# Optimization experiments

Measured on AMD Instinct MI355X. Metric: run time of the kernel, lower is better.

The kernel has to match this reference:

```python
import jax, jax.numpy as jnp
import numpy as np

BATCH = 1024
D = 256          # input_size == embed_size (forced by elementwise multiply)
NUM_REL = 42     # num_classes + 2
FEAT = 30


def setup_inputs() -> dict:
    key = jax.random.key(0)
    k_x, k_q, k_f, k_r = jax.random.split(key, 4)
    x = jax.random.normal(k_x, (BATCH, D), dtype=jnp.float32)
    x_mask = jnp.ones((BATCH,), dtype=bool)  # unused by the module body
    q = jax.random.randint(k_q, (BATCH, BATCH), 0, NUM_REL, dtype=jnp.int64)
    f = jax.random.normal(k_f, (BATCH, FEAT), dtype=jnp.float32)  # unused by the module body
    # relation embedding table, init std=0.001, row 0 zeroed (padding relation)
    R_emb = jax.random.normal(k_r, (NUM_REL, D), dtype=jnp.float32) * 0.001
    R_emb = R_emb.at[0].set(0.0)
    return {"x": x, "x_mask": x_mask, "q": q, "f": f, "R_emb": R_emb}


def reference(x, x_mask, q, f, R_emb):
    # r[i,j,d] = R_emb[q[i,j], d]   (the big O(B^2*D) gather)
    r = R_emb[q]  # [B, B, D]
    # attn[i,j] = sum_d r[i,j,d] * x[j,d] * x[i,d]
    attn = jnp.einsum('ijd,jd,id->ij', r, x, x)  # [B, B]
    weights = jax.nn.softmax(attn, axis=-1)
    outputs = weights @ x  # [B, D]
    return outputs
```

## Files before the change

kernel.cpp:

```cpp
#include <hip/hip_runtime.h>
#include <hip/hip_bf16.h>

#define BB 1024
#define DD 256
#define NREL 42
#define AST 264

typedef __attribute__((ext_vector_type(8))) short short8_t;
typedef __attribute__((ext_vector_type(4))) short short4_t;
typedef __attribute__((ext_vector_type(4))) float f32x4;
typedef __attribute__((ext_vector_type(4))) int   i32x4;
typedef __attribute__((ext_vector_type(4))) unsigned int u32x4;

__device__ __forceinline__ unsigned short bf16_of(float f) {
    unsigned u = __float_as_uint(f);
    return (unsigned short)((u + 0x7FFFu + ((u >> 16) & 1u)) >> 16);
}

__device__ __forceinline__ float blo(unsigned u) { return __uint_as_float(u << 16); }
__device__ __forceinline__ float bhi(unsigned u) { return __uint_as_float(u & 0xFFFF0000u); }

__device__ __forceinline__ void dot8bf4(u32x4 a0, u32x4 a1, u32x4 a2, u32x4 a3,
                                        u32x4 xv,
                                        float& r0, float& r1, float& r2, float& r3) {
    #pragma unroll
    for (int e = 0; e < 4; ++e) {
        const float xl = blo(xv[e]);
        const float xh = bhi(xv[e]);
        r0 = fmaf(blo(a0[e]), xl, r0);  r0 = fmaf(bhi(a0[e]), xh, r0);
        r1 = fmaf(blo(a1[e]), xl, r1);  r1 = fmaf(bhi(a1[e]), xh, r1);
        r2 = fmaf(blo(a2[e]), xl, r2);  r2 = fmaf(bhi(a2[e]), xh, r2);
        r3 = fmaf(blo(a3[e]), xl, r3);  r3 = fmaf(bhi(a3[e]), xh, r3);
    }
}

__global__ __launch_bounds__(256) void cvt_kernel(const float* __restrict__ x,
                                                  unsigned short* __restrict__ xh8,
                                                  unsigned short* __restrict__ xbfT) {
    __shared__ float t32[64][68];
    const int bj = blockIdx.x * 64;
    const int bd = blockIdx.y * 64;
    const int tid = threadIdx.x;
    const int tr = tid >> 4;
    const int tc = tid & 15;

    #pragma unroll
    for (int rr = 0; rr < 4; ++rr) {
        const int jl = rr * 16 + tr;
        const f32x4 v = *reinterpret_cast<const f32x4*>(&x[(bj + jl) * DD + bd + tc * 4]);
        *reinterpret_cast<f32x4*>(&t32[jl][tc * 4]) = v;
    }
    __syncthreads();

    #pragma unroll
    for (int rr = 0; rr < 4; ++rr) {
        const int dl = rr * 16 + tr;
        short4_t h;
        #pragma unroll
        for (int e = 0; e < 4; ++e) h[e] = (short)bf16_of(t32[tc * 4 + e][dl]);
        *reinterpret_cast<short4_t*>(&xbfT[(bd + dl) * BB + bj + tc * 4]) = h;
    }

    #pragma unroll
    for (int c = 0; c < 2; ++c) {
        const int idx = c * 256 + tid;
        const int jl  = idx & 63;
        const int d8l = idx >> 6;
        short8_t hv;
        #pragma unroll
        for (int e = 0; e < 8; ++e) hv[e] = (short)bf16_of(t32[jl][d8l * 8 + e]);
        *reinterpret_cast<short8_t*>(
            &xh8[(size_t)((bd >> 3) + d8l) * (BB * 8) + (bj + jl) * 8]) = hv;
    }
}

__global__ __launch_bounds__(1024) void attn_kernel(const float* __restrict__ x,
                                                    const int* __restrict__ q,
                                                    const float* __restrict__ R,
                                                    const unsigned short* __restrict__ xh8,
                                                    unsigned short* __restrict__ P) {
    __shared__ __align__(16) unsigned short Ah[4][NREL * AST];
    __shared__ float s_attn[4][BB];
    __shared__ unsigned short s_qs[4][BB];

    const int tid  = threadIdx.x;
    const int w    = tid >> 6;
    const int lane = tid & 63;
    const int i0   = blockIdx.x * 4;

    {
        const int r  = tid >> 8;
        const int c4 = (tid & 255) * 4;
        const int qi = i0 + r;
        const i32x4 qa = *reinterpret_cast<const i32x4*>(&q[qi * BB + c4]);
        short4_t sa;
        sa[0] = (short)qa[0]; sa[1] = (short)qa[1];
        sa[2] = (short)qa[2]; sa[3] = (short)qa[3];
        *reinterpret_cast<short4_t*>(&s_qs[r][c4]) = sa;
    }

    #pragma unroll
    for (int i2 = 0; i2 < 4; ++i2) {
        const int i = i0 + i2;
        for (int c = tid; c < NREL * 32; c += 1024) {
            const int k  = c >> 5;
            const int d0 = (c & 31) * 8;
            const f32x4 r0 = *reinterpret_cast<const f32x4*>(&R[k * DD + d0]);
            const f32x4 r1 = *reinterpret_cast<const f32x4*>(&R[k * DD + d0 + 4]);
            const f32x4 x0 = *reinterpret_cast<const f32x4*>(&x[i * DD + d0]);
            const f32x4 x1 = *reinterpret_cast<const f32x4*>(&x[i * DD + d0 + 4]);
            short8_t hv;
            #pragma unroll
            for (int e = 0; e < 4; ++e) {
                hv[e]     = (short)bf16_of(r0[e] * x0[e]);
                hv[e + 4] = (short)bf16_of(r1[e] * x1[e]);
            }
            *reinterpret_cast<short8_t*>(&Ah[i2][k * AST + d0]) = hv;
        }
    }

    __syncthreads();

    const int j0 = tid;
    const unsigned short* a0 = &Ah[0][(int)s_qs[0][j0] * AST];
    const unsigned short* a1 = &Ah[1][(int)s_qs[1][j0] * AST];
    const unsigned short* a2 = &Ah[2][(int)s_qs[2][j0] * AST];
    const unsigned short* a3 = &Ah[3][(int)s_qs[3][j0] * AST];
    const unsigned short* xp = xh8 + (size_t)j0 * 8;

    float c0 = 0.f, c1 = 0.f, c2 = 0.f, c3 = 0.f;

    #pragma unroll 2
    for (int d8 = 0; d8 < 32; ++d8) {
        const u32x4 xv = *reinterpret_cast<const u32x4*>(xp + (size_t)d8 * (BB * 8));

        const int ao = d8 * 8;
        const u32x4 av0 = *reinterpret_cast<const u32x4*>(a0 + ao);
        const u32x4 av1 = *reinterpret_cast<const u32x4*>(a1 + ao);
        const u32x4 av2 = *reinterpret_cast<const u32x4*>(a2 + ao);
        const u32x4 av3 = *reinterpret_cast<const u32x4*>(a3 + ao);

        dot8bf4(av0, av1, av2, av3, xv, c0, c1, c2, c3);
    }

    s_attn[0][j0] = c0;
    s_attn[1][j0] = c1;
    s_attn[2][j0] = c2;
    s_attn[3][j0] = c3;

    __syncthreads();

    const int p2 = w >> 2;
    const int jq = w & 3;
    const int i  = i0 + p2;

    f32x4 v4[4];
    #pragma unroll
    for (int kk = 0; kk < 4; ++kk)
        v4[kk] = *reinterpret_cast<const f32x4*>(&s_attn[p2][kk * 256 + lane * 4]);

    float m = -1e30f;
    #pragma unroll
    for (int kk = 0; kk < 4; ++kk)
        m = fmaxf(m, fmaxf(fmaxf(v4[kk][0], v4[kk][1]), fmaxf(v4[kk][2], v4[kk][3])));
    #pragma unroll
    for (int off = 1; off < 64; off <<= 1) m = fmaxf(m, __shfl_xor(m, off));

    float e[16];
    float ssum = 0.f;
    #pragma unroll
    for (int kk = 0; kk < 4; ++kk)
        #pragma unroll
        for (int ee = 0; ee < 4; ++ee) {
            const float t2 = __expf(v4[kk][ee] - m);
            e[kk * 4 + ee] = t2;
            ssum += t2;
        }
    #pragma unroll
    for (int off = 1; off < 64; off <<= 1) ssum += __shfl_xor(ssum, off);
    const float inv = 1.0f / ssum;

    {
        short4_t pv;
        #pragma unroll
        for (int ee = 0; ee < 4; ++ee) pv[ee] = (short)bf16_of(e[jq * 4 + ee] * inv);
        *reinterpret_cast<short4_t*>(&P[i * BB + jq * 256 + lane * 4]) = pv;
    }
}

__global__ __launch_bounds__(256) void out_partial(const unsigned short* __restrict__ P,
                                                   const unsigned short* __restrict__ xbfT,
                                                   float* __restrict__ part) {
    const int tid = threadIdx.x;
    const int wave = tid >> 6, lane = tid & 63;
    const int lcol = lane & 15;
    const int lk8  = (lane >> 4) * 8;
    const int i0 = blockIdx.y * 64 + wave * 16;
    const int d0 = blockIdx.x * 64;
    const int k0 = blockIdx.z * 256;

    f32x4 acc[4];
    #pragma unroll
    for (int nt = 0; nt < 4; ++nt) acc[nt] = (f32x4)0.0f;

    #pragma unroll
    for (int ks = 0; ks < 8; ++ks) {
        const short8_t a = *reinterpret_cast<const short8_t*>(
            &P[(i0 + lcol) * BB + k0 + ks * 32 + lk8]);
        #pragma unroll
        for (int nt = 0; nt < 4; ++nt) {
            const short8_t b = *reinterpret_cast<const short8_t*>(
                &xbfT[(d0 + nt * 16 + lcol) * BB + k0 + ks * 32 + lk8]);
            acc[nt] = __builtin_amdgcn_mfma_f32_16x16x32_bf16(a, b, acc[nt], 0, 0, 0);
        }
    }

    const int rbase = (lane >> 4) * 4;
    float* pz = part + (size_t)blockIdx.z * BB * DD;
    #pragma unroll
    for (int r = 0; r < 4; ++r)
        #pragma unroll
        for (int nt = 0; nt < 4; ++nt)
            pz[(i0 + rbase + r) * DD + d0 + nt * 16 + lcol] = acc[nt][r];
}

__global__ __launch_bounds__(256) void out_reduce(const float* __restrict__ part,
                                                  float* __restrict__ out) {
    const int idx = blockIdx.x * DD + threadIdx.x;
    out[idx] = (part[idx] + part[BB * DD + idx]) +
               (part[2 * BB * DD + idx] + part[3 * BB * DD + idx]);
}

extern "C" void kernel_launch(void* const* d_in, const int* in_sizes, int n_in,
                              void* d_out, int out_size, void* d_ws, size_t ws_size,
                              hipStream_t stream) {
    (void)in_sizes; (void)n_in; (void)out_size; (void)ws_size;
    const float* x = (const float*)d_in[0];
    const int* q = (const int*)d_in[2];
    const float* R = (const float*)d_in[4];
    float* out = (float*)d_out;

    char* ws = (char*)d_ws;
    unsigned short* xh8  = (unsigned short*)(ws);
    unsigned short* xbfT = (unsigned short*)(ws + (512u << 10));
    unsigned short* P    = (unsigned short*)(ws + (1024u << 10));
    float*          part = (float*)(ws + (3072u << 10));

    cvt_kernel<<<dim3(16, 4), 256, 0, stream>>>(x, xh8, xbfT);
    attn_kernel<<<dim3(256), 1024, 0, stream>>>(x, q, R, xh8, P);
    out_partial<<<dim3(4, 16, 4), 256, 0, stream>>>(P, xbfT, part);
    out_reduce<<<dim3(BB), 256, 0, stream>>>(part, out);
}
```

Measured before the change: 40.71 us.

## Process two query rows per attention block and split softmax across waves

The attention kernel now handles two rows per block instead of four, so it launches twice as many blocks and uses half the shared memory per block. The aim is more parallelism across the 256 compute units and more blocks resident at once. Each row's softmax is now spread over 8 waves, with cross-wave max and sum reductions through shared memory, adding two extra barriers. The trade-off is that every xh8 column load is reused for only two rows rather than four, which doubles global traffic for x and for the per-block Ah table setup.

```diff
diff --git a/kernel.cpp b/kernel.cpp
--- a/kernel.cpp
+++ b/kernel.cpp
@@ -8,8 +8,11 @@
 
 typedef __attribute__((ext_vector_type(8))) short short8_t;
 typedef __attribute__((ext_vector_type(4))) short short4_t;
+typedef __attribute__((ext_vector_type(2))) short short2_t;
 typedef __attribute__((ext_vector_type(4))) float f32x4;
+typedef __attribute__((ext_vector_type(2))) float f32x2;
 typedef __attribute__((ext_vector_type(4))) int   i32x4;
+typedef __attribute__((ext_vector_type(2))) int   i32x2;
 typedef __attribute__((ext_vector_type(4))) unsigned int u32x4;
 
 __device__ __forceinline__ unsigned short bf16_of(float f) {
@@ -20,17 +23,16 @@
 __device__ __forceinline__ float blo(unsigned u) { return __uint_as_float(u << 16); }
 __device__ __forceinline__ float bhi(unsigned u) { return __uint_as_float(u & 0xFFFF0000u); }
 
-__device__ __forceinline__ void dot8bf4(u32x4 a0, u32x4 a1, u32x4 a2, u32x4 a3,
-                                        u32x4 xv,
-                                        float& r0, float& r1, float& r2, float& r3) {
+__device__ __forceinline__ void dot8bf2(u32x4 aa, u32x4 ab, u32x4 xv,
+                                        float& ra, float& rb) {
     #pragma unroll
     for (int e = 0; e < 4; ++e) {
         const float xl = blo(xv[e]);
         const float xh = bhi(xv[e]);
-        r0 = fmaf(blo(a0[e]), xl, r0);  r0 = fmaf(bhi(a0[e]), xh, r0);
-        r1 = fmaf(blo(a1[e]), xl, r1);  r1 = fmaf(bhi(a1[e]), xh, r1);
-        r2 = fmaf(blo(a2[e]), xl, r2);  r2 = fmaf(bhi(a2[e]), xh, r2);
-        r3 = fmaf(blo(a3[e]), xl, r3);  r3 = fmaf(bhi(a3[e]), xh, r3);
+        ra = fmaf(blo(aa[e]), xl, ra);
+        ra = fmaf(bhi(aa[e]), xh, ra);
+        rb = fmaf(blo(ab[e]), xl, rb);
+        rb = fmaf(bhi(ab[e]), xh, rb);
     }
 }
 
@@ -79,28 +81,27 @@
                                                     const float* __restrict__ R,
                                                     const unsigned short* __restrict__ xh8,
                                                     unsigned short* __restrict__ P) {
-    __shared__ __align__(16) unsigned short Ah[4][NREL * AST];
-    __shared__ float s_attn[4][BB];
-    __shared__ unsigned short s_qs[4][BB];
+    __shared__ __align__(16) unsigned short Ah[2][NREL * AST];
+    __shared__ float s_attn[2][BB];
+    __shared__ unsigned short s_qs[2][BB];
+    __shared__ float red_m[2][8], red_s[2][8];
 
     const int tid  = threadIdx.x;
     const int w    = tid >> 6;
     const int lane = tid & 63;
-    const int i0   = blockIdx.x * 4;
+    const int i0   = blockIdx.x * 2;
 
     {
-        const int r  = tid >> 8;
-        const int c4 = (tid & 255) * 4;
-        const int qi = i0 + r;
-        const i32x4 qa = *reinterpret_cast<const i32x4*>(&q[qi * BB + c4]);
-        short4_t sa;
+        const int r  = tid >> 9;
+        const int c2 = (tid & 511) * 2;
+        const i32x2 qa = *reinterpret_cast<const i32x2*>(&q[(i0 + r) * BB + c2]);
+        short2_t sa;
         sa[0] = (short)qa[0]; sa[1] = (short)qa[1];
-        sa[2] = (short)qa[2]; sa[3] = (short)qa[3];
-        *reinterpret_cast<short4_t*>(&s_qs[r][c4]) = sa;
-    }
-
-    #pragma unroll
-    for (int i2 = 0; i2 < 4; ++i2) {
+        *reinterpret_cast<short2_t*>(&s_qs[r][c2]) = sa;
+    }
+
+    #pragma unroll
+    for (int i2 = 0; i2 < 2; ++i2) {
         const int i = i0 + i2;
         for (int c = tid; c < NREL * 32; c += 1024) {
             const int k  = c >> 5;
@@ -124,67 +125,56 @@
     const int j0 = tid;
     const unsigned short* a0 = &Ah[0][(int)s_qs[0][j0] * AST];
     const unsigned short* a1 = &Ah[1][(int)s_qs[1][j0] * AST];
-    const unsigned short* a2 = &Ah[2][(int)s_qs[2][j0] * AST];
-    const unsigned short* a3 = &Ah[3][(int)s_qs[3][j0] * AST];
     const unsigned short* xp = xh8 + (size_t)j0 * 8;
 
-    float c0 = 0.f, c1 = 0.f, c2 = 0.f, c3 = 0.f;
+    float c0 = 0.f, c1 = 0.f;
 
     #pragma unroll 2
     for (int d8 = 0; d8 < 32; ++d8) {
         const u32x4 xv = *reinterpret_cast<const u32x4*>(xp + (size_t)d8 * (BB * 8));
-
         const int ao = d8 * 8;
         const u32x4 av0 = *reinterpret_cast<const u32x4*>(a0 + ao);
         const u32x4 av1 = *reinterpret_cast<const u32x4*>(a1 + ao);
-        const u32x4 av2 = *reinterpret_cast<const u32x4*>(a2 + ao);
-        const u32x4 av3 = *reinterpret_cast<const u32x4*>(a3 + ao);
-
-        dot8bf4(av0, av1, av2, av3, xv, c0, c1, c2, c3);
+        dot8bf2(av0, av1, xv, c0, c1);
     }
 
     s_attn[0][j0] = c0;
     s_attn[1][j0] = c1;
-    s_attn[2][j0] = c2;
-    s_attn[3][j0] = c3;
-
-    __syncthreads();
-
-    const int p2 = w >> 2;
-    const int jq = w & 3;
-    const int i  = i0 + p2;
-
-    f32x4 v4[4];
-    #pragma unroll
-    for (int kk = 0; kk < 4; ++kk)
-        v4[kk] = *reinterpret_cast<const f32x4*>(&s_attn[p2][kk * 256 + lane * 4]);
-
-    float m = -1e30f;
-    #pragma unroll
-    for (int kk = 0; kk < 4; ++kk)
-        m = fmaxf(m, fmaxf(fmaxf(v4[kk][0], v4[kk][1]), fmaxf(v4[kk][2], v4[kk][3])));
+
+    __syncthreads();
+
+    const int r  = w >> 3;
+    const int s  = w & 7;
+    const int jb = s * 128 + lane * 2;
+    const int i  = i0 + r;
+
+    const f32x2 v = *reinterpret_cast<const f32x2*>(&s_attn[r][jb]);
+    float m = fmaxf(v[0], v[1]);
     #pragma unroll
     for (int off = 1; off < 64; off <<= 1) m = fmaxf(m, __shfl_xor(m, off));
-
-    float e[16];
-    float ssum = 0.f;
-    #pragma unroll
-    for (int kk = 0; kk < 4; ++kk)
-        #pragma unroll
-        for (int ee = 0; ee < 4; ++ee) {
-            const float t2 = __expf(v4[kk][ee] - m);
-            e[kk * 4 + ee] = t2;
-            ssum += t2;
-        }
+    if (lane == 0) red_m[r][s] = m;
+    __syncthreads();
+    m = red_m[r][0];
+    #pragma unroll
+    for (int e = 1; e < 8; ++e) m = fmaxf(m, red_m[r][e]);
+
+    const float e0 = __expf(v[0] - m);
+    const float e1 = __expf(v[1] - m);
+    float ssum = e0 + e1;
     #pragma unroll
     for (int off = 1; off < 64; off <<= 1) ssum += __shfl_xor(ssum, off);
+    if (lane == 0) red_s[r][s] = ssum;
+    __syncthreads();
+    ssum = 0.f;
+    #pragma unroll
+    for (int e = 1; e < 9; ++e) ssum += red_s[r][e - 1];
     const float inv = 1.0f / ssum;
 
     {
-        short4_t pv;
-        #pragma unroll
-        for (int ee = 0; ee < 4; ++ee) pv[ee] = (short)bf16_of(e[jq * 4 + ee] * inv);
-        *reinterpret_cast<short4_t*>(&P[i * BB + jq * 256 + lane * 4]) = pv;
+        short2_t pv;
+        pv[0] = (short)bf16_of(e0 * inv);
+        pv[1] = (short)bf16_of(e1 * inv);
+        *reinterpret_cast<short2_t*>(&P[i * BB + jb]) = pv;
     }
 }
 
@@ -247,7 +237,7 @@
     float*          part = (float*)(ws + (3072u << 10));
 
     cvt_kernel<<<dim3(16, 4), 256, 0, stream>>>(x, xh8, xbfT);
-    attn_kernel<<<dim3(256), 1024, 0, stream>>>(x, q, R, xh8, P);
+    attn_kernel<<<dim3(512), 1024, 0, stream>>>(x, q, R, xh8, P);
     out_partial<<<dim3(4, 16, 4), 256, 0, stream>>>(P, xbfT, part);
     out_reduce<<<dim3(BB), 256, 0, stream>>>(part, out);
 }
```

After: 41.83 us. 1.03x slower.
